# Kernel optimization log

Hardware: AMD Instinct MI355X
Metric: run time of the kernel (lower is better)

The kernel has to match this reference:

```python
import jax, jax.numpy as jnp
import numpy as np

WBITS = 4
GROUP_SIZE = 64
QMAX = 2 ** WBITS - 1  # 15
EPS = 1e-5


def setup_inputs() -> dict:
    key = jax.random.key(0)
    k1, k2, k3 = jax.random.split(key, 3)
    x = jax.random.normal(k1, (1, 512, 11008), dtype=jnp.float32)
    weight = jax.random.normal(k2, (4096, 11008), dtype=jnp.float32) * 0.02
    bias = jax.random.normal(k3, (4096,), dtype=jnp.float32) * 0.02
    return {"x": x, "weight": weight, "bias": bias}


def fake_quant_groupwise(w: jnp.ndarray) -> jnp.ndarray:
    """Uniform affine (asymmetric) group-wise fake quantization of the weight.

    Groups of GROUP_SIZE contiguous elements along the flattened weight share
    one (scale, zero_point) pair, computed dynamically from min/max per group,
    as in UniformAffineQuantizer(wbits, group_size, weight).
    """
    orig_shape = w.shape
    wg = w.reshape(-1, GROUP_SIZE)                     # [n_groups, G]
    xmin = jnp.min(wg, axis=1, keepdims=True)          # [n_groups, 1]
    xmax = jnp.max(wg, axis=1, keepdims=True)
    scale = jnp.maximum(xmax - xmin, EPS) / QMAX       # [n_groups, 1]
    zero_point = jnp.round(-xmin / scale)              # [n_groups, 1]
    w_int = jnp.clip(jnp.round(wg / scale) + zero_point, 0, QMAX)
    w_dq = (w_int - zero_point) * scale
    return w_dq.reshape(orig_shape)


def reference(x, weight, bias):
    w_q = fake_quant_groupwise(weight)                 # [out, in]
    # F.linear: x @ w_q.T + bias
    out = jnp.einsum('bsi,oi->bso', x, w_q) + bias
    return out
```

## Files before the change

kernel.cpp:

```cpp
#include <hip/hip_runtime.h>
#include <hip/hip_bf16.h>
#include <stdint.h>

typedef __attribute__((ext_vector_type(8))) short bf16x8;
typedef __attribute__((ext_vector_type(8))) short short8;
typedef __attribute__((ext_vector_type(4))) float f32x4;

#define M_DIM 512
#define N_DIM 4096
#define K_DIM 11008
#define KSTEPS 172

#define GLOBAL_AS(p) ((const __attribute__((address_space(1))) void*)(p))
#define LDS_AS(p)    ((__attribute__((address_space(3))) void*)(p))

__device__ __forceinline__ short f2bf(float f) {
    unsigned u = __float_as_uint(f);
    unsigned r = u + 0x7fff + ((u >> 16) & 1);
    return (short)(r >> 16);
}

__device__ __forceinline__ unsigned cvt_pk_bf16(float lo, float hi) {
    unsigned r;
    asm("v_cvt_pk_bf16_f32 %0, %1, %2" : "=v"(r) : "v"(lo), "v"(hi));
    return r;
}

__device__ __forceinline__ float dpp_xor1(float v) {
    return __int_as_float(__builtin_amdgcn_mov_dpp(__float_as_int(v), 0xB1, 0xf, 0xf, true));
}
__device__ __forceinline__ float dpp_xor2(float v) {
    return __int_as_float(__builtin_amdgcn_mov_dpp(__float_as_int(v), 0x4E, 0xf, 0xf, true));
}

__device__ __forceinline__ void fence_bar() {
    asm volatile("" ::: "memory");
    __builtin_amdgcn_s_barrier();
    asm volatile("" ::: "memory");
}
#define LGKM0() asm volatile("s_waitcnt lgkmcnt(0)" ::: "memory")
#define VMCNT(n) asm volatile("s_waitcnt vmcnt(" #n ")" ::: "memory")

__global__ __launch_bounds__(256) void conv_x(const float* __restrict__ x, short* __restrict__ xb) {
    const long long total = (long long)M_DIM * K_DIM;
    for (long long e0 = ((long long)blockIdx.x * 256 + threadIdx.x) * 8;
         e0 < total;
         e0 += (long long)gridDim.x * 256 * 8) {
        const float4* p = (const float4*)(x + e0);
        float4 v0 = p[0];
        float4 v1 = p[1];
        short8 s;
        s[0] = f2bf(v0.x); s[1] = f2bf(v0.y); s[2] = f2bf(v0.z); s[3] = f2bf(v0.w);
        s[4] = f2bf(v1.x); s[5] = f2bf(v1.y); s[6] = f2bf(v1.z); s[7] = f2bf(v1.w);
        *(short8*)(xb + e0) = s;
    }
}


template<int QD>
__device__ __forceinline__ void phase_reads(const short* __restrict__ Asd,
                                            const short* __restrict__ Bsd,
                                            int arow, int brow, int qb,
                                            bf16x8 (&af)[2][2], bf16x8 (&bfr)[2][4]) {
    if (QD == 0) {
        #pragma unroll
        for (int ks = 0; ks < 2; ++ks)
            #pragma unroll
            for (int fn = 0; fn < 4; ++fn) {
                const int r = brow + fn * 16;
                bfr[ks][fn] = *(const bf16x8*)&Bsd[r * 64 + (((ks * 4 + qb) ^ (r & 7)) * 8)];
            }
    }
    #pragma unroll
    for (int ks = 0; ks < 2; ++ks)
        #pragma unroll
        for (int j = 0; j < 2; ++j) {
            const int r = arow + (QD * 2 + j) * 16;
            af[ks][j] = *(const bf16x8*)&Asd[r * 64 + (((ks * 4 + qb) ^ (r & 7)) * 8)];
        }
}

template<int QD>
__device__ __forceinline__ void phase_mfma(const bf16x8 (&af)[2][2], const bf16x8 (&bfr)[2][4],
                                           f32x4 (&acc)[8][4]) {
    __builtin_amdgcn_s_setprio(1);
    #pragma unroll
    for (int ks = 0; ks < 2; ++ks)
        #pragma unroll
        for (int j = 0; j < 2; ++j)
            #pragma unroll
            for (int fn = 0; fn < 4; ++fn)
                acc[QD * 2 + j][fn] = __builtin_amdgcn_mfma_f32_16x16x32_bf16(
                    af[ks][j], bfr[ks][fn], acc[QD * 2 + j][fn], 0, 0, 0);
    __builtin_amdgcn_s_setprio(0);
}

__global__ __launch_bounds__(512, 2) void gemm_fq(const short* __restrict__ A,
                                                  const float* __restrict__ W,
                                                  unsigned short* __restrict__ P,
                                                  int spb) {
    __shared__ short As[2][256 * 64];
    __shared__ short Bs[2][256 * 64];
    const int tid  = threadIdx.x;
    const int lane = tid & 63;
    const int w    = tid >> 6;
    const int wr   = w >> 2;
    const int wc   = w & 3;
    const int m0   = blockIdx.y * 256;
    const int n0   = blockIdx.x * 256;
    const int kt0  = blockIdx.z * spb;
    const int kt1  = min(kt0 + spb, KSTEPS);

    const int srow = tid >> 3;
    const int sswz = (tid & 7) ^ (srow & 7);
    const int rC   = tid >> 2;
    const int qC   = tid & 3;
    const int arow = wr * 128 + (lane & 15);
    const int brow = wc * 64 + (lane & 15);
    const int qb   = lane >> 4;

    f32x4  acc[8][4] = {};
    bf16x8 bfr[2][4];
    bf16x8 af[2][2];
    float4 C0[4], C1[4];

    auto stageA = [&](int d, int h, int kt) {
        #pragma unroll
        for (int l = 0; l < 2; ++l) {
            __builtin_amdgcn_global_load_lds(
                GLOBAL_AS(A + (size_t)(m0 + h * 128 + l * 64 + srow) * K_DIM + kt * 64 + sswz * 8),
                LDS_AS(&As[d][(h * 128 + l * 64 + w * 8) * 64]), 16, 0, 0);
        }
    };
    auto loadC = [&](float4 (&dst)[4], int c, int kt) {
        const float4* src = (const float4*)(W + (size_t)(n0 + c * 128 + rC) * K_DIM + (size_t)kt * 64 + qC * 16);
        #pragma unroll
        for (int j = 0; j < 4; ++j) dst[j] = src[j];
    };
    auto quantC = [&](const float4 (&v)[4], int c, short* BsF) {
        const float* pv = (const float*)&v[0];
        float mns[8], mxs[8];
        #pragma unroll
        for (int j = 0; j < 8; ++j) {
            mns[j] = fminf(pv[2 * j], pv[2 * j + 1]);
            mxs[j] = fmaxf(pv[2 * j], pv[2 * j + 1]);
        }
        #pragma unroll
        for (int st = 4; st >= 1; st >>= 1)
            #pragma unroll
            for (int j = 0; j < st; ++j) {
                mns[j] = fminf(mns[j], mns[j + st]);
                mxs[j] = fmaxf(mxs[j], mxs[j + st]);
            }
        float mn = fminf(mns[0], dpp_xor1(mns[0]));
        mn = fminf(mn, dpp_xor2(mn));
        float mx = fmaxf(mxs[0], dpp_xor1(mxs[0]));
        mx = fmaxf(mx, dpp_xor2(mx));
        float range = fmaxf(mx - mn, 1e-5f);
        float scale = range * (1.0f / 15.0f);
        float rs    = 1.0f / scale;
        const int r    = c * 128 + rC;
        const int base = r * 64;
        #pragma unroll
        for (int s4 = 0; s4 < 2; ++s4) {
            float q[8];
            #pragma unroll
            for (int j = 0; j < 8; ++j)
                q[j] = rintf(pv[s4 * 8 + j] * rs) * scale;
            union { unsigned u[4]; short8 s; } pk;
            #pragma unroll
            for (int j = 0; j < 4; ++j)
                pk.u[j] = cvt_pk_bf16(q[2 * j], q[2 * j + 1]);
            const int s = qC * 2 + s4;
            *(short8*)&BsF[base + ((s ^ (r & 7)) * 8)] = pk.s;
        }
    };

    loadC(C0, 0, kt0);
    loadC(C1, 1, kt0);
    stageA(0, 0, kt0);
    stageA(0, 1, kt0);
    VMCNT(8);  quantC(C0, 0, Bs[0]);
    VMCNT(4);  quantC(C1, 1, Bs[0]);
    loadC(C0, 0, kt0 + 1);
    loadC(C1, 1, kt0 + 1);
    VMCNT(8);
    LGKM0();
    fence_bar();

    int par = 0;
    for (int t = kt0; t < kt1; ++t) {
        const int tn  = (t + 1 < kt1) ? t + 1 : t;
        const int tn2 = (t + 2 < kt1) ? t + 2 : kt1 - 1;
        const short* Asc = As[par];
        const short* Bsc = Bs[par];
        short* Bsn = Bs[par ^ 1];
        phase_reads<0>(Asc, Bsc, arow, brow, qb, af, bfr);
        VMCNT(4);
        quantC(C0, 0, Bsn);
        stageA(par ^ 1, 0, tn);
        fence_bar(); LGKM0();
        phase_mfma<0>(af, bfr, acc);
        fence_bar();
        phase_reads<1>(Asc, Bsc, arow, brow, qb, af, bfr);
        VMCNT(2);
        quantC(C1, 1, Bsn);
        stageA(par ^ 1, 1, tn);
        fence_bar(); LGKM0();
        phase_mfma<1>(af, bfr, acc);
        fence_bar();
        phase_reads<2>(Asc, Bsc, arow, brow, qb, af, bfr);
        loadC(C0, 0, tn2);
        fence_bar(); LGKM0();
        phase_mfma<2>(af, bfr, acc);
        fence_bar();
        phase_reads<3>(Asc, Bsc, arow, brow, qb, af, bfr);
        loadC(C1, 1, tn2);
        fence_bar(); LGKM0();
        phase_mfma<3>(af, bfr, acc);
        VMCNT(8);
        fence_bar();
        par ^= 1;
    }

    VMCNT(0);

    unsigned short* out = P + (size_t)blockIdx.z * M_DIM * N_DIM;
    #pragma unroll
    for (int fm = 0; fm < 8; ++fm) {
        #pragma unroll
        for (int fn = 0; fn < 4; ++fn) {
            const int col  = n0 + wc * 64 + fn * 16 + (lane & 15);
            const int rowb = m0 + wr * 128 + fm * 16 + (lane >> 4) * 4;
            #pragma unroll
            for (int r = 0; r < 4; ++r) {
                out[(size_t)(rowb + r) * N_DIM + col] = (unsigned short)f2bf(acc[fm][fn][r]);
            }
        }
    }
}

__global__ __launch_bounds__(256) void reduce_out(const unsigned short* __restrict__ P,
                                                  const float* __restrict__ bias,
                                                  float* __restrict__ out,
                                                  int splitk) {
    const size_t total = (size_t)M_DIM * N_DIM;
    for (size_t idx8 = ((size_t)blockIdx.x * 256 + threadIdx.x) * 8;
         idx8 < total;
         idx8 += (size_t)gridDim.x * 256 * 8) {
        const int col = (int)(idx8 % N_DIM);
        float s[8];
        {
            float4 b0 = *(const float4*)(bias + col);
            float4 b1 = *(const float4*)(bias + col + 4);
            s[0] = b0.x; s[1] = b0.y; s[2] = b0.z; s[3] = b0.w;
            s[4] = b1.x; s[5] = b1.y; s[6] = b1.z; s[7] = b1.w;
        }
        for (int sp = 0; sp < splitk; ++sp) {
            short8 p = *(const short8*)(P + (size_t)sp * total + idx8);
            #pragma unroll
            for (int j = 0; j < 8; ++j)
                s[j] += __uint_as_float(((unsigned)(unsigned short)p[j]) << 16);
        }
        float4 o0 = {s[0], s[1], s[2], s[3]};
        float4 o1 = {s[4], s[5], s[6], s[7]};
        *(float4*)(out + idx8) = o0;
        *(float4*)(out + idx8 + 4) = o1;
    }
}

extern "C" void kernel_launch(void* const* d_in, const int* in_sizes, int n_in,
                              void* d_out, int out_size, void* d_ws, size_t ws_size,
                              hipStream_t stream) {
    const float* x    = (const float*)d_in[0];
    const float* wgt  = (const float*)d_in[1];
    const float* bias = (const float*)d_in[2];
    float* out = (float*)d_out;

    char* ws = (char*)d_ws;
    const size_t xb_bytes = (size_t)M_DIM * K_DIM * 2;
    short* xb = (short*)ws;
    unsigned short* part = (unsigned short*)(ws + xb_bytes);

    const size_t per_split = (size_t)M_DIM * N_DIM * 2;
    size_t avail = (ws_size > xb_bytes) ? (ws_size - xb_bytes) : 0;
    int splitk = 1, spb = KSTEPS;
    for (int sk = 8; sk >= 1; --sk) {
        if ((size_t)sk * per_split > avail) continue;
        int s = (KSTEPS + sk - 1) / sk;
        int last = KSTEPS - (sk - 1) * s;
        if (last < 2) continue;
        splitk = sk; spb = s;
        break;
    }

    hipLaunchKernelGGL(conv_x, dim3(2048), dim3(256), 0, stream, x, xb);
    hipLaunchKernelGGL(gemm_fq, dim3(N_DIM / 256, M_DIM / 256, splitk), dim3(512), 0, stream,
                       xb, wgt, part, spb);
    hipLaunchKernelGGL(reduce_out, dim3(1024), dim3(256), 0, stream, part, bias, out, splitk);
}
```

Baseline: 98.61 us.

## Replace four-phase interleaved main loop with a single compute-then-prefetch block

This drops the four-phase schedule, which interleaved LDS reads, MFMA batches, weight quantization and A staging with barriers and priority hints between phases. Each iteration now reads all B fragments and runs all MFMAs in one block. It then quantizes both weight chunks, stages the next A tile, issues the next weight loads, and synchronizes once. The aim is to cut barrier and waitcnt overhead and give the compiler a freer schedule. The cost is that quantization VALU work and global loads no longer overlap with the MFMA work.

```diff
diff --git a/kernel.cpp b/kernel.cpp
--- a/kernel.cpp
+++ b/kernel.cpp
@@ -54,45 +54,6 @@
         s[4] = f2bf(v1.x); s[5] = f2bf(v1.y); s[6] = f2bf(v1.z); s[7] = f2bf(v1.w);
         *(short8*)(xb + e0) = s;
     }
-}
-
-
-template<int QD>
-__device__ __forceinline__ void phase_reads(const short* __restrict__ Asd,
-                                            const short* __restrict__ Bsd,
-                                            int arow, int brow, int qb,
-                                            bf16x8 (&af)[2][2], bf16x8 (&bfr)[2][4]) {
-    if (QD == 0) {
-        #pragma unroll
-        for (int ks = 0; ks < 2; ++ks)
-            #pragma unroll
-            for (int fn = 0; fn < 4; ++fn) {
-                const int r = brow + fn * 16;
-                bfr[ks][fn] = *(const bf16x8*)&Bsd[r * 64 + (((ks * 4 + qb) ^ (r & 7)) * 8)];
-            }
-    }
-    #pragma unroll
-    for (int ks = 0; ks < 2; ++ks)
-        #pragma unroll
-        for (int j = 0; j < 2; ++j) {
-            const int r = arow + (QD * 2 + j) * 16;
-            af[ks][j] = *(const bf16x8*)&Asd[r * 64 + (((ks * 4 + qb) ^ (r & 7)) * 8)];
-        }
-}
-
-template<int QD>
-__device__ __forceinline__ void phase_mfma(const bf16x8 (&af)[2][2], const bf16x8 (&bfr)[2][4],
-                                           f32x4 (&acc)[8][4]) {
-    __builtin_amdgcn_s_setprio(1);
-    #pragma unroll
-    for (int ks = 0; ks < 2; ++ks)
-        #pragma unroll
-        for (int j = 0; j < 2; ++j)
-            #pragma unroll
-            for (int fn = 0; fn < 4; ++fn)
-                acc[QD * 2 + j][fn] = __builtin_amdgcn_mfma_f32_16x16x32_bf16(
-                    af[ks][j], bfr[ks][fn], acc[QD * 2 + j][fn], 0, 0, 0);
-    __builtin_amdgcn_s_setprio(0);
 }
 
 __global__ __launch_bounds__(512, 2) void gemm_fq(const short* __restrict__ A,
@@ -120,8 +81,6 @@
     const int qb   = lane >> 4;
 
     f32x4  acc[8][4] = {};
-    bf16x8 bfr[2][4];
-    bf16x8 af[2][2];
     float4 C0[4], C1[4];
 
     auto stageA = [&](int d, int h, int kt) {
@@ -195,30 +154,42 @@
         const short* Asc = As[par];
         const short* Bsc = Bs[par];
         short* Bsn = Bs[par ^ 1];
-        phase_reads<0>(Asc, Bsc, arow, brow, qb, af, bfr);
-        VMCNT(4);
+
+        bf16x8 bfr[2][4];
+        #pragma unroll
+        for (int ks = 0; ks < 2; ++ks)
+            #pragma unroll
+            for (int fn = 0; fn < 4; ++fn) {
+                const int r = brow + fn * 16;
+                bfr[ks][fn] = *(const bf16x8*)&Bsc[r * 64 + (((ks * 4 + qb) ^ (r & 7)) * 8)];
+            }
+        #pragma unroll
+        for (int qd = 0; qd < 4; ++qd) {
+            bf16x8 af[2][2];
+            #pragma unroll
+            for (int ks = 0; ks < 2; ++ks)
+                #pragma unroll
+                for (int j = 0; j < 2; ++j) {
+                    const int r = arow + (qd * 2 + j) * 16;
+                    af[ks][j] = *(const bf16x8*)&Asc[r * 64 + (((ks * 4 + qb) ^ (r & 7)) * 8)];
+                }
+            #pragma unroll
+            for (int ks = 0; ks < 2; ++ks)
+                #pragma unroll
+                for (int j = 0; j < 2; ++j)
+                    #pragma unroll
+                    for (int fn = 0; fn < 4; ++fn)
+                        acc[qd * 2 + j][fn] = __builtin_amdgcn_mfma_f32_16x16x32_bf16(
+                            af[ks][j], bfr[ks][fn], acc[qd * 2 + j][fn], 0, 0, 0);
+        }
         quantC(C0, 0, Bsn);
+        quantC(C1, 1, Bsn);
         stageA(par ^ 1, 0, tn);
-        fence_bar(); LGKM0();
-        phase_mfma<0>(af, bfr, acc);
-        fence_bar();
-        phase_reads<1>(Asc, Bsc, arow, brow, qb, af, bfr);
-        VMCNT(2);
-        quantC(C1, 1, Bsn);
         stageA(par ^ 1, 1, tn);
-        fence_bar(); LGKM0();
-        phase_mfma<1>(af, bfr, acc);
-        fence_bar();
-        phase_reads<2>(Asc, Bsc, arow, brow, qb, af, bfr);
         loadC(C0, 0, tn2);
-        fence_bar(); LGKM0();
-        phase_mfma<2>(af, bfr, acc);
-        fence_bar();
-        phase_reads<3>(Asc, Bsc, arow, brow, qb, af, bfr);
         loadC(C1, 1, tn2);
-        fence_bar(); LGKM0();
-        phase_mfma<3>(af, bfr, acc);
         VMCNT(8);
+        LGKM0();
         fence_bar();
         par ^= 1;
     }
```

New measurement: 92.32 us. -6.4%, faster.
